# Kernel optimization log

Measured on AMD Instinct MI355X. Metric: run time of the kernel, lower is better.

Reference implementation:

```python
import jax, jax.numpy as jnp
import numpy as np

EPS = 1e-5
NUM_HEADS = 4


def _layer_norm(x, g, b):
    m = jnp.mean(x, axis=-1, keepdims=True)
    v = jnp.mean((x - m) ** 2, axis=-1, keepdims=True)
    return (x - m) / jnp.sqrt(v + EPS) * g + b


def setup_inputs() -> dict:
    key = jax.random.key(0)
    ks = jax.random.split(key, 32)
    B, N, ND, TD, L = 100000, 20, 128, 64, 2
    HD = 128  # num_heads * attention_dim
    CD = ND + TD  # 192
    s = 0.02
    inp = {
        "node_features": jax.random.normal(ks[0], (B, ND), jnp.float32),
        "neighbor_features": jax.random.normal(ks[1], (B, N, ND), jnp.float32),
        "node_times": jax.random.uniform(ks[2], (B,), jnp.float32),
        "neighbor_times": jax.random.uniform(ks[3], (B, N), jnp.float32),
        "time_freq": jax.random.normal(ks[4], (TD,), jnp.float32),
        "time_phase": jnp.zeros((TD,), jnp.float32),
        "Wq": jax.random.normal(ks[5], (L, CD, HD), jnp.float32) * s,
        "bq": jnp.zeros((L, HD), jnp.float32),
        "Wk": jax.random.normal(ks[6], (L, CD, HD), jnp.float32) * s,
        "bk": jnp.zeros((L, HD), jnp.float32),
        "Wv": jax.random.normal(ks[7], (L, CD, HD), jnp.float32) * s,
        "bv": jnp.zeros((L, HD), jnp.float32),
        "Wo": jax.random.normal(ks[8], (L, HD, ND), jnp.float32) * s,
        "bo": jnp.zeros((L, ND), jnp.float32),
        "W1": jax.random.normal(ks[9], (L, ND, 2 * ND), jnp.float32) * s,
        "b1": jnp.zeros((L, 2 * ND), jnp.float32),
        "W2": jax.random.normal(ks[10], (L, 2 * ND, ND), jnp.float32) * s,
        "b2": jnp.zeros((L, ND), jnp.float32),
        "g1": jnp.ones((L, ND), jnp.float32),
        "be1": jnp.zeros((L, ND), jnp.float32),
        "g2": jnp.ones((L, ND), jnp.float32),
        "be2": jnp.zeros((L, ND), jnp.float32),
        "Wc1": jax.random.normal(ks[11], (ND, ND // 2), jnp.float32) * s,
        "bc1": jnp.zeros((ND // 2,), jnp.float32),
        "Wc2": jax.random.normal(ks[12], (ND // 2, 1), jnp.float32) * s,
        "bc2": jnp.zeros((1,), jnp.float32),
        "mask": jax.random.randint(ks[13], (B, N), 0, 2, jnp.int32),
    }
    return inp


def reference(node_features, neighbor_features, node_times, neighbor_times,
              time_freq, time_phase, Wq, bq, Wk, bk, Wv, bv, Wo, bo,
              W1, b1, W2, b2, g1, be1, g2, be2, Wc1, bc1, Wc2, bc2, mask):
    L, _, HD = Wq.shape
    B, N, ND = neighbor_features.shape
    H = NUM_HEADS
    D = HD // H
    scale = 1.0 / np.sqrt(D).astype(np.float32)
    # time encodings (Bochner): cos(t * w + phi)
    tq = jnp.cos(node_times[:, None] * time_freq + time_phase)          # [B, TD]
    tk = jnp.cos(neighbor_times[..., None] * time_freq + time_phase)   # [B, N, TD]
    kcomb = jnp.concatenate([neighbor_features, tk], axis=-1)           # [B, N, CD]
    pad = (mask == 0)[:, None, :]                                       # [B, 1, N]
    x = node_features
    for l in range(L):
        qcomb = jnp.concatenate([x, tq], axis=-1)                       # [B, CD]
        q = (qcomb @ Wq[l] + bq[l]).reshape(B, H, D)
        k = (kcomb @ Wk[l] + bk[l]).reshape(B, N, H, D)
        v = (kcomb @ Wv[l] + bv[l]).reshape(B, N, H, D)
        scores = jnp.einsum('bhd,bnhd->bhn', q, k) * scale              # [B, H, N]
        scores = jnp.where(pad, jnp.float32(-1e9), scores)
        w = jax.nn.softmax(scores, axis=-1)
        a = jnp.einsum('bhn,bnhd->bhd', w, v).reshape(B, HD)
        attn = a @ Wo[l] + bo[l]                                        # [B, ND]
        x = _layer_norm(x + attn, g1[l], be1[l])
        ff = jax.nn.relu(x @ W1[l] + b1[l]) @ W2[l] + b2[l]
        x = _layer_norm(x + ff, g2[l], be2[l])
    h = jax.nn.relu(x @ Wc1 + bc1)
    return jax.nn.sigmoid(h @ Wc2 + bc2)                                # [B, 1]
```

## Files before the change

### kernel.cpp

```cpp
#include <hip/hip_runtime.h>

#define BB 100000
#define NN 20
#define ND 128
#define TD 64
#define CD 192
#define HD 128
#define NH 4
#define DH 32
#define NL 2

typedef __attribute__((ext_vector_type(8))) short bf16x8;
typedef __attribute__((ext_vector_type(4))) float f32x4;

static __device__ __forceinline__ float bf2f(unsigned short u) {
  return __uint_as_float(((unsigned)u) << 16);
}
static __device__ __forceinline__ unsigned short f2bf(float x) {
  unsigned b = __float_as_uint(x);
  return (unsigned short)((b + 0x7FFFu + ((b >> 16) & 1u)) >> 16);
}
static __device__ __forceinline__ bf16x8 load_a8(const float* p) {
  float4 a = *(const float4*)p, b = *(const float4*)(p + 4);
  bf16x8 r;
  r[0] = (short)f2bf(a.x); r[1] = (short)f2bf(a.y);
  r[2] = (short)f2bf(a.z); r[3] = (short)f2bf(a.w);
  r[4] = (short)f2bf(b.x); r[5] = (short)f2bf(b.y);
  r[6] = (short)f2bf(b.z); r[7] = (short)f2bf(b.w);
  return r;
}


__global__ __launch_bounds__(256) void conv_w(
    const float* __restrict__ Wq, const float* __restrict__ Wk,
    const float* __restrict__ Wv, const float* __restrict__ Wo,
    const float* __restrict__ W1, const float* __restrict__ W2,
    unsigned short* __restrict__ WF) {
  int t = blockIdx.x;
  int l = t / 304, tt = t % 304;
#pragma unroll
  for (int e = 0; e < 2; ++e) {
    int idx = threadIdx.x * 2 + e;
    int lane = idx >> 3, j = idx & 7;
    int wk = ((lane >> 4) << 3) + j;
    int c16 = lane & 15;
    float v;
    if (tt < 48) {
      int kt = tt >> 3, n2 = tt & 7;
      v = Wq[((size_t)l * CD + kt * 32 + wk) * HD + n2 * 16 + c16];
    } else if (tt < 96) {
      int t2 = tt - 48; int h = t2 / 12, n2 = t2 % 12;
      v = Wk[((size_t)l * CD + n2 * 16 + c16) * HD + h * 32 + wk];
    } else if (tt < 144) {
      int t2 = tt - 96; int h = t2 / 12, r2 = t2 % 12, kt = r2 >> 1, n2 = r2 & 1;
      v = Wv[((size_t)l * CD + kt * 32 + wk) * HD + h * 32 + n2 * 16 + c16];
    } else if (tt < 176) {
      int t2 = tt - 144; int kt = t2 >> 3, n2 = t2 & 7;
      v = Wo[((size_t)l * HD + kt * 32 + wk) * ND + n2 * 16 + c16];
    } else if (tt < 240) {
      int t2 = tt - 176; int kt = t2 >> 4, n2 = t2 & 15;
      v = W1[((size_t)l * ND + kt * 32 + wk) * (2 * ND) + n2 * 16 + c16];
    } else {
      int t2 = tt - 240; int kt = t2 >> 3, n2 = t2 & 7;
      v = W2[((size_t)l * 2 * ND + kt * 32 + wk) * ND + n2 * 16 + c16];
    }
    WF[(size_t)l * 155648 + (size_t)tt * 512 + idx] = f2bf(v);
  }
}

__global__ __launch_bounds__(256) void prep_tq(
    const float* __restrict__ ntime, const float* __restrict__ tf,
    const float* __restrict__ tp, float* __restrict__ tqf) {
  int i = blockIdx.x * 256 + threadIdx.x;
  int b = i >> 6, j = i & 63;
  tqf[i] = __cosf(ntime[b] * tf[j] + tp[j]);
}

__global__ __launch_bounds__(256) void prep_mb(const int* __restrict__ mask,
                                               unsigned* __restrict__ mb) {
  int e = blockIdx.x * 256 + threadIdx.x;
  if (e < BB) {
    unsigned m = 0;
    for (int n = 0; n < NN; ++n)
      m |= (mask[(size_t)e * NN + n] != 0 ? 1u : 0u) << n;
    mb[e] = m;
  }
}

__global__ __launch_bounds__(256) void gemm_yr(
    const float* __restrict__ A, const float* __restrict__ tqf,
    const unsigned short* __restrict__ WFl, const float* __restrict__ bq,
    unsigned short* __restrict__ rb) {
  __shared__ unsigned short ylds[16][136];
  const int tid = threadIdx.x;
  const int wv = tid >> 6, lane = tid & 63;
  const int m0 = blockIdx.x << 4;
  const int arow = m0 + (lane & 15);
  const int kgrp = (lane >> 4) << 3;
  {
    f32x4 acc[2];
    acc[0] = f32x4{0.f, 0.f, 0.f, 0.f};
    acc[1] = f32x4{0.f, 0.f, 0.f, 0.f};
    for (int kt = 0; kt < 6; ++kt) {
      bf16x8 af = (kt < 4)
                      ? load_a8(A + (size_t)arow * ND + kt * 32 + kgrp)
                      : load_a8(tqf + (size_t)arow * TD + (kt - 4) * 32 + kgrp);
#pragma unroll
      for (int i = 0; i < 2; ++i) {
        int nt = wv + 4 * i;
        bf16x8 bf = *(const bf16x8*)(WFl + (((size_t)(kt * 8 + nt)) << 9) +
                                     (lane << 3));
        acc[i] = __builtin_amdgcn_mfma_f32_16x16x32_bf16(af, bf, acc[i], 0, 0, 0);
      }
    }
    int lrow = (lane >> 4) << 2;
#pragma unroll
    for (int i = 0; i < 2; ++i) {
      int col = (wv + 4 * i) * 16 + (lane & 15);
      float bv = bq[col];
#pragma unroll
      for (int rr = 0; rr < 4; ++rr)
        ylds[lrow + rr][col] = f2bf(acc[i][rr] + bv);
    }
  }
  __syncthreads();
  {
    f32x4 acc[12];
#pragma unroll
    for (int i = 0; i < 12; ++i) acc[i] = f32x4{0.f, 0.f, 0.f, 0.f};
    bf16x8 af = *(const bf16x8*)&ylds[lane & 15][wv * 32 + kgrp];
    const unsigned short* B = WFl + 24576 + (size_t)wv * 12 * 512;
#pragma unroll
    for (int i = 0; i < 12; ++i) {
      bf16x8 bf = *(const bf16x8*)(B + (((size_t)i) << 9) + (lane << 3));
      acc[i] = __builtin_amdgcn_mfma_f32_16x16x32_bf16(af, bf, acc[i], 0, 0, 0);
    }
    int crow = m0 + ((lane >> 4) << 2);
#pragma unroll
    for (int i = 0; i < 12; ++i) {
      int col = wv * 192 + i * 16 + (lane & 15);
#pragma unroll
      for (int rr = 0; rr < 4; ++rr)
        rb[(size_t)(crow + rr) * 768 + col] = f2bf(acc[i][rr]);
    }
  }
}

__global__ __launch_bounds__(256) void gemm_aln1ff1(
    const unsigned short* __restrict__ u, const unsigned short* __restrict__ WFl,
    const float* __restrict__ bv, const float* __restrict__ bo,
    const float* __restrict__ res, const float* __restrict__ gamma,
    const float* __restrict__ beta, const float* __restrict__ b1,
    float* __restrict__ xout, unsigned short* __restrict__ h1b) {
  __shared__ unsigned short alds[16][136];
  __shared__ float Cs[16][132];
  const int tid = threadIdx.x;
  const int wv = tid >> 6, lane = tid & 63;
  const int m0 = blockIdx.x << 4;
  const int arow = m0 + (lane & 15);
  const int kgrp = (lane >> 4) << 3;
  {
    f32x4 acc0 = {0.f, 0.f, 0.f, 0.f}, acc1 = {0.f, 0.f, 0.f, 0.f};
    const unsigned short* B = WFl + 49152 + (size_t)wv * 12 * 512;
    for (int kt = 0; kt < 6; ++kt) {
      bf16x8 af = *(const bf16x8*)(u + (size_t)arow * 768 + wv * 192 +
                                   kt * 32 + kgrp);
      bf16x8 b0 = *(const bf16x8*)(B + (((size_t)(kt * 2 + 0)) << 9) + (lane << 3));
      bf16x8 b1f = *(const bf16x8*)(B + (((size_t)(kt * 2 + 1)) << 9) + (lane << 3));
      acc0 = __builtin_amdgcn_mfma_f32_16x16x32_bf16(af, b0, acc0, 0, 0, 0);
      acc1 = __builtin_amdgcn_mfma_f32_16x16x32_bf16(af, b1f, acc1, 0, 0, 0);
    }
    int lrow = (lane >> 4) << 2;
    int c0 = wv * 32 + (lane & 15), c1 = wv * 32 + 16 + (lane & 15);
    float bv0 = bv[c0], bv1 = bv[c1];
#pragma unroll
    for (int rr = 0; rr < 4; ++rr) {
      alds[lrow + rr][c0] = f2bf(acc0[rr] + bv0);
      alds[lrow + rr][c1] = f2bf(acc1[rr] + bv1);
    }
  }
  __syncthreads();
  {
    const int nt0 = wv, nt1 = wv + 4;
    f32x4 acc0 = {0.f, 0.f, 0.f, 0.f}, acc1 = {0.f, 0.f, 0.f, 0.f};
    for (int kt = 0; kt < 4; ++kt) {
      bf16x8 af = *(const bf16x8*)&alds[lane & 15][kt * 32 + kgrp];
      bf16x8 b0 = *(const bf16x8*)(WFl + 73728 +
                                   (((size_t)(kt * 8 + nt0)) << 9) + (lane << 3));
      bf16x8 b1f = *(const bf16x8*)(WFl + 73728 +
                                    (((size_t)(kt * 8 + nt1)) << 9) + (lane << 3));
      acc0 = __builtin_amdgcn_mfma_f32_16x16x32_bf16(af, b0, acc0, 0, 0, 0);
      acc1 = __builtin_amdgcn_mfma_f32_16x16x32_bf16(af, b1f, acc1, 0, 0, 0);
    }
    {
      int lrow = (lane >> 4) << 2;
      int c0 = nt0 * 16 + (lane & 15), c1 = nt1 * 16 + (lane & 15);
      float bv0 = bo[c0], bv1 = bo[c1];
#pragma unroll
      for (int rr = 0; rr < 4; ++rr) {
        Cs[lrow + rr][c0] = acc0[rr] + bv0;
        Cs[lrow + rr][c1] = acc1[rr] + bv1;
      }
    }
    __syncthreads();
#pragma unroll
    for (int rr = 0; rr < 4; ++rr) {
      int rw = wv * 4 + rr;
      size_t grow = (size_t)(m0 + rw) * ND;
      float y0 = Cs[rw][lane] + res[grow + lane];
      float y1 = Cs[rw][lane + 64] + res[grow + lane + 64];
      float s = y0 + y1, ss = y0 * y0 + y1 * y1;
#pragma unroll
      for (int off = 32; off > 0; off >>= 1) {
        s += __shfl_xor(s, off);
        ss += __shfl_xor(ss, off);
      }
      float mean = s * (1.f / ND);
      float var = ss * (1.f / ND) - mean * mean;
      float rstd = rsqrtf(var + 1e-5f);
      float x0 = (y0 - mean) * rstd * gamma[lane] + beta[lane];
      float x1 = (y1 - mean) * rstd * gamma[lane + 64] + beta[lane + 64];
      xout[grow + lane] = x0;
      xout[grow + lane + 64] = x1;
      Cs[rw][lane] = x0;
      Cs[rw][lane + 64] = x1;
    }
  }
  __syncthreads();
  {
    f32x4 acc[4];
#pragma unroll
    for (int i = 0; i < 4; ++i) acc[i] = f32x4{0.f, 0.f, 0.f, 0.f};
    for (int kt = 0; kt < 4; ++kt) {
      bf16x8 af = load_a8(&Cs[lane & 15][kt * 32 + kgrp]);
#pragma unroll
      for (int i = 0; i < 4; ++i) {
        int nt = wv + 4 * i;
        bf16x8 bf = *(const bf16x8*)(WFl + 90112 +
                                     (((size_t)(kt * 16 + nt)) << 9) + (lane << 3));
        acc[i] = __builtin_amdgcn_mfma_f32_16x16x32_bf16(af, bf, acc[i], 0, 0, 0);
      }
    }
    int crow = m0 + ((lane >> 4) << 2);
#pragma unroll
    for (int i = 0; i < 4; ++i) {
      int col = (wv + 4 * i) * 16 + (lane & 15);
      float bvv = b1[col];
#pragma unroll
      for (int rr = 0; rr < 4; ++rr)
        h1b[(size_t)(crow + rr) * (2 * ND) + col] =
            f2bf(fmaxf(acc[i][rr] + bvv, 0.f));
    }
  }
}

template <int ABF, int CLS>
__global__ __launch_bounds__(256) void gemm_ln(
    const void* __restrict__ A, int lda, int ktiles,
    const unsigned short* __restrict__ BF,
    const float* __restrict__ bias, const float* __restrict__ res,
    const float* __restrict__ gamma, const float* __restrict__ beta,
    float* __restrict__ xout,
    const float* __restrict__ Wc1, const float* __restrict__ bc1,
    const float* __restrict__ Wc2, const float* __restrict__ bc2,
    float* __restrict__ out) {
  __shared__ float Cs[16][132];
  __shared__ float hsh[CLS ? 16 : 1][64];
  const int tid = threadIdx.x;
  const int wv = tid >> 6, lane = tid & 63;
  const int m0 = blockIdx.x << 4;
  const int arow = m0 + (lane & 15);
  const int kgrp = (lane >> 4) << 3;
  const int nt0 = wv, nt1 = wv + 4;
  f32x4 acc0 = {0.f, 0.f, 0.f, 0.f}, acc1 = {0.f, 0.f, 0.f, 0.f};
  for (int kt = 0; kt < ktiles; ++kt) {
    bf16x8 af;
    if (ABF)
      af = *(const bf16x8*)((const unsigned short*)A + (size_t)arow * lda +
                            kt * 32 + kgrp);
    else
      af = load_a8((const float*)A + (size_t)arow * lda + kt * 32 + kgrp);
    bf16x8 b0 = *(const bf16x8*)(BF + (((size_t)(kt * 8 + nt0)) << 9) + (lane << 3));
    bf16x8 b1 = *(const bf16x8*)(BF + (((size_t)(kt * 8 + nt1)) << 9) + (lane << 3));
    acc0 = __builtin_amdgcn_mfma_f32_16x16x32_bf16(af, b0, acc0, 0, 0, 0);
    acc1 = __builtin_amdgcn_mfma_f32_16x16x32_bf16(af, b1, acc1, 0, 0, 0);
  }
  {
    const int lrow = (lane >> 4) << 2;
    int c0 = nt0 * 16 + (lane & 15), c1 = nt1 * 16 + (lane & 15);
    float bv0 = bias[c0], bv1 = bias[c1];
#pragma unroll
    for (int rr = 0; rr < 4; ++rr) {
      Cs[lrow + rr][c0] = acc0[rr] + bv0;
      Cs[lrow + rr][c1] = acc1[rr] + bv1;
    }
  }
  __syncthreads();
#pragma unroll
  for (int rr = 0; rr < 4; ++rr) {
    int rw = wv * 4 + rr;
    size_t grow = (size_t)(m0 + rw) * ND;
    float y0 = Cs[rw][lane] + res[grow + lane];
    float y1 = Cs[rw][lane + 64] + res[grow + lane + 64];
    float s = y0 + y1, ss = y0 * y0 + y1 * y1;
#pragma unroll
    for (int off = 32; off > 0; off >>= 1) {
      s += __shfl_xor(s, off);
      ss += __shfl_xor(ss, off);
    }
    float mean = s * (1.f / ND);
    float var = ss * (1.f / ND) - mean * mean;
    float rstd = rsqrtf(var + 1e-5f);
    float x0 = (y0 - mean) * rstd * gamma[lane] + beta[lane];
    float x1 = (y1 - mean) * rstd * gamma[lane + 64] + beta[lane + 64];
    if (CLS) {
      Cs[rw][lane] = x0;
      Cs[rw][lane + 64] = x1;
    } else {
      xout[grow + lane] = x0;
      xout[grow + lane + 64] = x1;
    }
  }
  if (CLS) {
    __syncthreads();
#pragma unroll
    for (int rep = 0; rep < 4; ++rep) {
      int idx = rep * 256 + tid;
      int row = idx >> 6, j = idx & 63;
      float a = 0.f;
      for (int c = 0; c < ND; ++c) a += Cs[row][c] * Wc1[c * 64 + j];
      hsh[row][j] = fmaxf(a + bc1[j], 0.f);
    }
    __syncthreads();
#pragma unroll
    for (int rr = 0; rr < 4; ++rr) {
      int row = wv * 4 + rr;
      float p = hsh[row][lane] * Wc2[lane];
#pragma unroll
      for (int off = 32; off > 0; off >>= 1) p += __shfl_xor(p, off);
      if (lane == 0)
        out[m0 + row] = 1.f / (1.f + expf(-(p + bc2[0])));
    }
  }
}

__global__ __launch_bounds__(256) void attn_b(
    const float* __restrict__ nbf, const float* __restrict__ nbt,
    const float* __restrict__ tf, const float* __restrict__ tp,
    const unsigned* __restrict__ mb, const unsigned short* __restrict__ r,
    unsigned short* __restrict__ u) {
  __shared__ __align__(16) unsigned short kcb[2][NN][200];
  __shared__ __align__(16) float rs[2][768];
  __shared__ __align__(16) float scs[2][NH][NN];
  __shared__ unsigned msks[2];
  const int tid = threadIdx.x;
  const size_t e0 = (size_t)blockIdx.x * 2;

  if (tid < 192) {
    uint4 v = *(const uint4*)(r + e0 * 768 + tid * 8);
    const unsigned short* pv = (const unsigned short*)&v;
    float* dst = &rs[0][0] + tid * 8;
#pragma unroll
    for (int k = 0; k < 8; ++k) dst[k] = bf2f(pv[k]);
  }
  for (int i = tid; i < 2 * NN * 32; i += 256) {
    int el = i / (NN * 32), rem = i % (NN * 32);
    int n = rem >> 5, cq = rem & 31;
    float4 v = *(const float4*)&nbf[((e0 + el) * NN + n) * ND + cq * 4];
    ushort4 o;
    o.x = f2bf(v.x); o.y = f2bf(v.y); o.z = f2bf(v.z); o.w = f2bf(v.w);
    *(ushort4*)&kcb[el][n][cq * 4] = o;
  }
  for (int i = tid; i < 2 * NN * 32; i += 256) {
    int el = i / (NN * 32), rem = i % (NN * 32);
    int n = rem >> 5, jp = (rem & 31) * 2;
    float t = nbt[(e0 + el) * NN + n];
    unsigned a = f2bf(__cosf(t * tf[jp] + tp[jp]));
    unsigned b = f2bf(__cosf(t * tf[jp + 1] + tp[jp + 1]));
    *(unsigned*)&kcb[el][n][ND + jp] = a | (b << 16);
  }
  if (tid < 2) msks[tid] = mb[e0 + tid];
  __syncthreads();
  if (tid < 2 * NH * NN) {
    int el = tid / (NH * NN), rem = tid % (NH * NN);
    int h = rem / NN, n = rem % NN;
    const float* rp = &rs[el][h * CD];
    const unsigned short* kp = &kcb[el][n][0];
    float acc = 0.f;
    for (int c = 0; c < CD; c += 4) {
      float4 rv = *(const float4*)&rp[c];
      ushort4 kv = *(const ushort4*)&kp[c];
      acc += rv.x * bf2f(kv.x) + rv.y * bf2f(kv.y) + rv.z * bf2f(kv.z) +
             rv.w * bf2f(kv.w);
    }
    scs[el][h][n] =
        ((msks[el] >> n) & 1u) ? acc * 0.17677669529663687f : -1e9f;
  }
  __syncthreads();
  if (tid < 2 * NH) {
    int el = tid >> 2, h = tid & 3;
    float mx = -3.4e38f;
#pragma unroll
    for (int n = 0; n < NN; ++n) mx = fmaxf(mx, scs[el][h][n]);
    float ev[NN], s = 0.f;
#pragma unroll
    for (int n = 0; n < NN; ++n) { ev[n] = __expf(scs[el][h][n] - mx); s += ev[n]; }
    float inv = 1.f / s;
#pragma unroll
    for (int n = 0; n < NN; ++n) scs[el][h][n] = ev[n] * inv;
  }
  __syncthreads();
  for (int i = tid; i < 2 * NH * (CD / 4); i += 256) {
    int el = i / (NH * 48), rem = i % (NH * 48);
    int h = rem / 48, cq = (rem % 48) * 4;
    float a0 = 0.f, a1 = 0.f, a2 = 0.f, a3 = 0.f;
#pragma unroll
    for (int n = 0; n < NN; ++n) {
      float w = scs[el][h][n];
      ushort4 kv = *(const ushort4*)&kcb[el][n][cq];
      a0 += w * bf2f(kv.x); a1 += w * bf2f(kv.y);
      a2 += w * bf2f(kv.z); a3 += w * bf2f(kv.w);
    }
    ushort4 o;
    o.x = f2bf(a0); o.y = f2bf(a1); o.z = f2bf(a2); o.w = f2bf(a3);
    *(ushort4*)&u[(e0 + el) * 768 + h * CD + cq] = o;
  }
}

#define G 2
#define T 256
#define KCS 196
#define RUS 772

__global__ __launch_bounds__(T, 4) void tgat_fused(
    const float* __restrict__ nf, const float* __restrict__ nbf,
    const float* __restrict__ nt, const float* __restrict__ nbt,
    const float* __restrict__ tf, const float* __restrict__ tp,
    const float* __restrict__ Wq, const float* __restrict__ bq,
    const float* __restrict__ Wk,
    const float* __restrict__ Wv, const float* __restrict__ bv,
    const float* __restrict__ Wo, const float* __restrict__ bo,
    const float* __restrict__ W1, const float* __restrict__ b1,
    const float* __restrict__ W2, const float* __restrict__ b2,
    const float* __restrict__ g1, const float* __restrict__ be1,
    const float* __restrict__ g2, const float* __restrict__ be2,
    const float* __restrict__ Wc1, const float* __restrict__ bc1,
    const float* __restrict__ Wc2, const float* __restrict__ bc2,
    const int* __restrict__ mask,
    float* __restrict__ out) {
  __shared__ __align__(16) unsigned short kc[G][NN][KCS];
  __shared__ __align__(16) float xs[G][ND];
  __shared__ __align__(16) float tqs[G][TD];
  __shared__ __align__(16) float ys[G][HD];
  __shared__ __align__(16) float rus[G][RUS];
  __shared__ __align__(16) float scs[G][NH][NN];
  __shared__ __align__(16) float h1s[G][2 * ND];
  __shared__ __align__(16) unsigned msks[G];
  float* asv = &h1s[0][0];
  const int tid = threadIdx.x;
  const int b0 = blockIdx.x * G;
  {
    int g = tid >> 7, j = tid & 127;
    xs[g][j] = nf[(b0 + g) * ND + j];
  }
  if (tid < G * TD) {
    int g = tid >> 6, j = tid & 63;
    tqs[g][j] = __cosf(nt[b0 + g] * tf[j] + tp[j]);
  }
  if (tid < G) {
    unsigned m = 0;
    for (int n = 0; n < NN; ++n)
      m |= (mask[(b0 + tid) * NN + n] != 0 ? 1u : 0u) << n;
    msks[tid] = m;
  }
  for (int idx = tid; idx < G * NN * (ND / 4); idx += T) {
    int g = idx / (NN * 32), rem = idx % (NN * 32);
    int n = rem >> 5, cq = rem & 31;
    float4 v = *(const float4*)&nbf[(((b0 + g) * NN + n) * ND) + cq * 4];
    ushort4 o;
    o.x = f2bf(v.x); o.y = f2bf(v.y); o.z = f2bf(v.z); o.w = f2bf(v.w);
    *(ushort4*)&kc[g][n][cq * 4] = o;
  }
  for (int idx = tid; idx < G * NN * TD; idx += T) {
    int g = idx / (NN * TD), rem = idx % (NN * TD);
    int n = rem >> 6, j = rem & 63;
    kc[g][n][ND + j] = f2bf(__cosf(nbt[(b0 + g) * NN + n] * tf[j] + tp[j]));
  }
  __syncthreads();
  const float scale = 0.17677669529663687f;
  for (int l = 0; l < NL; ++l) {
    {
      int g = tid >> 7, j = tid & 127;
      const float* wq = Wq + (l * CD) * HD + j;
      float acc = bq[l * HD + j];
      for (int c = 0; c < CD; c += 4) {
        float4 qv = (c < ND) ? *(const float4*)&xs[g][c]
                             : *(const float4*)&tqs[g][c - ND];
        acc += qv.x * wq[(c + 0) * HD] + qv.y * wq[(c + 1) * HD] +
               qv.z * wq[(c + 2) * HD] + qv.w * wq[(c + 3) * HD];
      }
      ys[g][j] = acc;
    }
    __syncthreads();
    for (int rep = 0; rep < 3; ++rep) {
      int i = rep * T + tid;
      int h = i / CD;
      int c2 = i - h * CD;
      const float* wk = Wk + (l * CD + c2) * HD + h * DH;
      const float* yp0 = &ys[0][h * DH];
      const float* yp1 = &ys[1][h * DH];
      float a0 = 0.f, a1 = 0.f;
#pragma unroll
      for (int d = 0; d < DH; d += 4) {
        float4 w4 = *(const float4*)&wk[d];
        float4 y0 = *(const float4*)&yp0[d];
        float4 y1 = *(const float4*)&yp1[d];
        a0 += y0.x * w4.x + y0.y * w4.y + y0.z * w4.z + y0.w * w4.w;
        a1 += y1.x * w4.x + y1.y * w4.y + y1.z * w4.z + y1.w * w4.w;
      }
      rus[0][i] = a0;
      rus[1][i] = a1;
    }
    __syncthreads();
    if (tid < G * NH * NN) {
      int g = tid / (NH * NN), rem = tid % (NH * NN);
      int h = rem / NN, n = rem % NN;
      const float* rp = &rus[g][h * CD];
      const unsigned short* kp = &kc[g][n][0];
      float acc = 0.f;
      for (int c = 0; c < CD; c += 4) {
        float4 rv = *(const float4*)&rp[c];
        ushort4 kv = *(const ushort4*)&kp[c];
        acc += rv.x * bf2f(kv.x) + rv.y * bf2f(kv.y) + rv.z * bf2f(kv.z) +
               rv.w * bf2f(kv.w);
      }
      scs[g][h][n] = ((msks[g] >> n) & 1u) ? acc * scale : -1e9f;
    }
    __syncthreads();
    if (tid < G * NH) {
      int g = tid / NH, h = tid % NH;
      float mx = -3.4e38f;
#pragma unroll
      for (int n = 0; n < NN; ++n) mx = fmaxf(mx, scs[g][h][n]);
      float ev[NN], s = 0.f;
#pragma unroll
      for (int n = 0; n < NN; ++n) { ev[n] = __expf(scs[g][h][n] - mx); s += ev[n]; }
      float inv = 1.f / s;
#pragma unroll
      for (int n = 0; n < NN; ++n) scs[g][h][n] = ev[n] * inv;
    }
    __syncthreads();
    for (int flat = tid; flat < G * NH * (CD / 4); flat += T) {
      int g = flat / (NH * 48), iq = flat % (NH * 48);
      int h = iq / 48, c = (iq % 48) * 4;
      const unsigned short* kp = &kc[g][0][0];
      float a0 = 0.f, a1 = 0.f, a2 = 0.f, a3 = 0.f;
#pragma unroll
      for (int n = 0; n < NN; ++n) {
        float w = scs[g][h][n];
        ushort4 kv = *(const ushort4*)&kp[n * KCS + c];
        a0 += w * bf2f(kv.x); a1 += w * bf2f(kv.y);
        a2 += w * bf2f(kv.z); a3 += w * bf2f(kv.w);
      }
      *(float4*)&rus[g][h * CD + c] = make_float4(a0, a1, a2, a3);
    }
    __syncthreads();
    {
      int j = tid & (HD - 1);
      int g = tid >> 7;
      int h = j >> 5;
      const float* wv = Wv + (l * CD) * HD + j;
      float acc = 0.f;
      for (int c = 0; c < CD; c += 4) {
        float4 uv = *(const float4*)&rus[g][h * CD + c];
        acc += uv.x * wv[(c + 0) * HD] + uv.y * wv[(c + 1) * HD] +
               uv.z * wv[(c + 2) * HD] + uv.w * wv[(c + 3) * HD];
      }
      asv[g * HD + j] = acc + bv[l * HD + j];
    }
    __syncthreads();
    {
      int j = tid & (ND - 1);
      int g = tid >> 7;
      const float* wo = Wo + (l * HD) * ND + j;
      float acc = 0.f;
      for (int c = 0; c < HD; c += 4) {
        float4 av = *(const float4*)&asv[g * HD + c];
        acc += av.x * wo[(c + 0) * ND] + av.y * wo[(c + 1) * ND] +
               av.z * wo[(c + 2) * ND] + av.w * wo[(c + 3) * ND];
      }
      rus[g][j] = acc + bo[l * ND + j];
    }
    __syncthreads();
    if (tid < G * 64) {
      int g = tid >> 6, lane = tid & 63;
      float y0 = xs[g][lane] + rus[g][lane];
      float y1 = xs[g][lane + 64] + rus[g][lane + 64];
      float s = y0 + y1, ss = y0 * y0 + y1 * y1;
#pragma unroll
      for (int off = 32; off > 0; off >>= 1) {
        s += __shfl_xor(s, off);
        ss += __shfl_xor(ss, off);
      }
      float mean = s * (1.f / ND);
      float var = ss * (1.f / ND) - mean * mean;
      float rstd = rsqrtf(var + 1e-5f);
      xs[g][lane] = (y0 - mean) * rstd * g1[l * ND + lane] + be1[l * ND + lane];
      xs[g][lane + 64] =
          (y1 - mean) * rstd * g1[l * ND + lane + 64] + be1[l * ND + lane + 64];
    }
    __syncthreads();
    {
      int j = tid;
      const float* w1p = W1 + (l * ND) * (2 * ND) + j;
      float acc0 = 0.f, acc1 = 0.f;
      for (int c = 0; c < ND; c += 4) {
        float w0 = w1p[(c + 0) * 2 * ND], wa = w1p[(c + 1) * 2 * ND],
              w2 = w1p[(c + 2) * 2 * ND], w3 = w1p[(c + 3) * 2 * ND];
        float4 x0 = *(const float4*)&xs[0][c];
        float4 x1 = *(const float4*)&xs[1][c];
        acc0 += x0.x * w0 + x0.y * wa + x0.z * w2 + x0.w * w3;
        acc1 += x1.x * w0 + x1.y * wa + x1.z * w2 + x1.w * w3;
      }
      float b1v = b1[l * 2 * ND + j];
      h1s[0][j] = fmaxf(acc0 + b1v, 0.f);
      h1s[1][j] = fmaxf(acc1 + b1v, 0.f);
    }
    __syncthreads();
    {
      int j = tid & (ND - 1);
      int g = tid >> 7;
      const float* w2p = W2 + (l * 2 * ND) * ND + j;
      float acc = 0.f;
      for (int c = 0; c < 2 * ND; c += 4) {
        float4 hv = *(const float4*)&h1s[g][c];
        acc += hv.x * w2p[(c + 0) * ND] + hv.y * w2p[(c + 1) * ND] +
               hv.z * w2p[(c + 2) * ND] + hv.w * w2p[(c + 3) * ND];
      }
      rus[g][j] = acc + b2[l * ND + j];
    }
    __syncthreads();
    if (tid < G * 64) {
      int g = tid >> 6, lane = tid & 63;
      float y0 = xs[g][lane] + rus[g][lane];
      float y1 = xs[g][lane + 64] + rus[g][lane + 64];
      float s = y0 + y1, ss = y0 * y0 + y1 * y1;
#pragma unroll
      for (int off = 32; off > 0; off >>= 1) {
        s += __shfl_xor(s, off);
        ss += __shfl_xor(ss, off);
      }
      float mean = s * (1.f / ND);
      float var = ss * (1.f / ND) - mean * mean;
      float rstd = rsqrtf(var + 1e-5f);
      xs[g][lane] = (y0 - mean) * rstd * g2[l * ND + lane] + be2[l * ND + lane];
      xs[g][lane + 64] =
          (y1 - mean) * rstd * g2[l * ND + lane + 64] + be2[l * ND + lane + 64];
    }
    __syncthreads();
  }
  if (tid < G * 64) {
    int j = tid & 63;
    int g = tid >> 6;
    const float* wc = Wc1 + j;
    float acc = 0.f;
    for (int c = 0; c < ND; c += 4) {
      float4 xv = *(const float4*)&xs[g][c];
      acc += xv.x * wc[(c + 0) * 64] + xv.y * wc[(c + 1) * 64] +
             xv.z * wc[(c + 2) * 64] + xv.w * wc[(c + 3) * 64];
    }
    ((float*)scs)[g * 64 + j] = fmaxf(acc + bc1[j], 0.f);
  }
  __syncthreads();
  if (tid < G * 64) {
    int g = tid >> 6, lane = tid & 63;
    float p = ((float*)scs)[g * 64 + lane] * Wc2[lane];
#pragma unroll
    for (int off = 32; off > 0; off >>= 1) p += __shfl_xor(p, off);
    if (lane == 0) {
      float z = p + bc2[0];
      out[b0 + g] = 1.f / (1.f + expf(-z));
    }
  }
}

extern "C" void kernel_launch(void* const* d_in, const int* in_sizes, int n_in,
                              void* d_out, int out_size, void* d_ws,
                              size_t ws_size, hipStream_t stream) {
  (void)in_sizes; (void)n_in; (void)out_size;
  const float* nf  = (const float*)d_in[0];
  const float* nbf = (const float*)d_in[1];
  const float* ntm = (const float*)d_in[2];
  const float* nbt = (const float*)d_in[3];
  const float* tf  = (const float*)d_in[4];
  const float* tp  = (const float*)d_in[5];
  const float* Wq  = (const float*)d_in[6];
  const float* bq  = (const float*)d_in[7];
  const float* Wk  = (const float*)d_in[8];
  const float* Wv  = (const float*)d_in[10];
  const float* bv  = (const float*)d_in[11];
  const float* Wo  = (const float*)d_in[12];
  const float* bo  = (const float*)d_in[13];
  const float* W1  = (const float*)d_in[14];
  const float* b1  = (const float*)d_in[15];
  const float* W2  = (const float*)d_in[16];
  const float* b2  = (const float*)d_in[17];
  const float* g1  = (const float*)d_in[18];
  const float* be1 = (const float*)d_in[19];
  const float* g2  = (const float*)d_in[20];
  const float* be2 = (const float*)d_in[21];
  const float* Wc1 = (const float*)d_in[22];
  const float* bc1 = (const float*)d_in[23];
  const float* Wc2 = (const float*)d_in[24];
  const float* bc2 = (const float*)d_in[25];
  const int* mask  = (const int*)d_in[26];
  float* out = (float*)d_out;

  const size_t NEED = 282622592ull;
  if (ws_size >= NEED) {
    char* w = (char*)d_ws;
    unsigned short* WF = (unsigned short*)w;
    unsigned* mb = (unsigned*)(w + 622592);
    float* tqf = (float*)(w + 1022592);
    unsigned short* rb = (unsigned short*)(w + 26622592);
    unsigned short* h1b = (unsigned short*)(w + 180222592);
    float* xfb = (float*)(w + 231422592);

    conv_w<<<608, 256, 0, stream>>>(Wq, Wk, Wv, Wo, W1, W2, WF);
    prep_tq<<<25000, 256, 0, stream>>>(ntm, tf, tp, tqf);
    prep_mb<<<(BB + 255) / 256, 256, 0, stream>>>(mask, mb);

    const float* xsrc = nf;
    for (int l = 0; l < NL; ++l) {
      const unsigned short* WFl = WF + (size_t)l * 155648;
      gemm_yr<<<6250, 256, 0, stream>>>(xsrc, tqf, WFl, bq + l * HD, rb);
      attn_b<<<50000, 256, 0, stream>>>(nbf, nbt, tf, tp, mb, rb, rb);
      gemm_aln1ff1<<<6250, 256, 0, stream>>>(
          rb, WFl, bv + l * HD, bo + l * ND, xsrc, g1 + l * ND, be1 + l * ND,
          b1 + l * 2 * ND, xfb, h1b);
      if (l == NL - 1)
        gemm_ln<1, 1><<<6250, 256, 0, stream>>>(
            h1b, 2 * ND, 8, WFl + 122880, b2 + l * ND, xfb, g2 + l * ND,
            be2 + l * ND, xfb, Wc1, bc1, Wc2, bc2, out);
      else
        gemm_ln<1, 0><<<6250, 256, 0, stream>>>(
            h1b, 2 * ND, 8, WFl + 122880, b2 + l * ND, xfb, g2 + l * ND,
            be2 + l * ND, xfb, nullptr, nullptr, nullptr, nullptr, nullptr);
      xsrc = xfb;
    }
  } else {
    tgat_fused<<<BB / G, T, 0, stream>>>(nf, nbf, ntm, nbt, tf, tp, Wq, bq, Wk,
                                         Wv, bv, Wo, bo, W1, b1, W2, b2, g1,
                                         be1, g2, be2, Wc1, bc1, Wc2, bc2,
                                         mask, out);
  }
}
```

Baseline: 1.288 ms.

## Fuse Q projection, neighbor attention and output/FFN1 into one layer kernel

Merges gemm_yr, attn_b and gemm_aln1ff1 into a single per-layer kernel. The 768-wide projected query buffer and the attention output now stay in shared memory instead of making round trips through global memory. The time-encoding buffer for nodes is also stored as bf16 rather than fp32, which shrinks the workspace. In exchange, the fused kernel uses far more shared memory and handles attention serially in four groups of four rows with many barriers. That may cut occupancy and reduce how well neighbor loads overlap with compute.

New measurement: 1.928 ms. +49.7%, slower.

```diff
diff --git a/kernel.cpp b/kernel.cpp
--- a/kernel.cpp
+++ b/kernel.cpp
@@ -70,10 +70,10 @@
 
 __global__ __launch_bounds__(256) void prep_tq(
     const float* __restrict__ ntime, const float* __restrict__ tf,
-    const float* __restrict__ tp, float* __restrict__ tqf) {
+    const float* __restrict__ tp, unsigned short* __restrict__ tqb) {
   int i = blockIdx.x * 256 + threadIdx.x;
   int b = i >> 6, j = i & 63;
-  tqf[i] = __cosf(ntime[b] * tf[j] + tp[j]);
+  tqb[i] = f2bf(__cosf(ntime[b] * tf[j] + tp[j]));
 }
 
 __global__ __launch_bounds__(256) void prep_mb(const int* __restrict__ mask,
@@ -87,16 +87,28 @@
   }
 }
 
-__global__ __launch_bounds__(256) void gemm_yr(
-    const float* __restrict__ A, const float* __restrict__ tqf,
+__global__ __launch_bounds__(256) void layer_fused(
+    const float* __restrict__ A, const unsigned short* __restrict__ tqb,
     const unsigned short* __restrict__ WFl, const float* __restrict__ bq,
-    unsigned short* __restrict__ rb) {
-  __shared__ unsigned short ylds[16][136];
+    const float* __restrict__ nbf, const float* __restrict__ nbt,
+    const float* __restrict__ tf, const float* __restrict__ tp,
+    const unsigned* __restrict__ mb, const float* __restrict__ bv,
+    const float* __restrict__ bo, const float* __restrict__ gamma,
+    const float* __restrict__ beta, const float* __restrict__ b1,
+    float* __restrict__ xout, unsigned short* __restrict__ h1b) {
+  __shared__ __align__(16) unsigned short ylds[16][136];
+  __shared__ __align__(16) unsigned short rlds[16][768];
+  __shared__ __align__(16) unsigned short kcb[4][NN][200];
+  __shared__ __align__(16) float scs[4][NH][NN];
+  __shared__ __align__(16) unsigned short alds[16][136];
+  __shared__ __align__(16) float Cs[16][132];
+  __shared__ unsigned msks[4];
   const int tid = threadIdx.x;
   const int wv = tid >> 6, lane = tid & 63;
   const int m0 = blockIdx.x << 4;
   const int arow = m0 + (lane & 15);
   const int kgrp = (lane >> 4) << 3;
+
   {
     f32x4 acc[2];
     acc[0] = f32x4{0.f, 0.f, 0.f, 0.f};
@@ -104,7 +116,8 @@
     for (int kt = 0; kt < 6; ++kt) {
       bf16x8 af = (kt < 4)
                       ? load_a8(A + (size_t)arow * ND + kt * 32 + kgrp)
-                      : load_a8(tqf + (size_t)arow * TD + (kt - 4) * 32 + kgrp);
+                      : *(const bf16x8*)(tqb + (size_t)arow * TD +
+                                         (kt - 4) * 32 + kgrp);
 #pragma unroll
       for (int i = 0; i < 2; ++i) {
         int nt = wv + 4 * i;
@@ -117,10 +130,10 @@
 #pragma unroll
     for (int i = 0; i < 2; ++i) {
       int col = (wv + 4 * i) * 16 + (lane & 15);
-      float bv = bq[col];
+      float bvv = bq[col];
 #pragma unroll
       for (int rr = 0; rr < 4; ++rr)
-        ylds[lrow + rr][col] = f2bf(acc[i][rr] + bv);
+        ylds[lrow + rr][col] = f2bf(acc[i][rr] + bvv);
     }
   }
   __syncthreads();
@@ -135,36 +148,88 @@
       bf16x8 bf = *(const bf16x8*)(B + (((size_t)i) << 9) + (lane << 3));
       acc[i] = __builtin_amdgcn_mfma_f32_16x16x32_bf16(af, bf, acc[i], 0, 0, 0);
     }
-    int crow = m0 + ((lane >> 4) << 2);
+    int lrow = (lane >> 4) << 2;
 #pragma unroll
     for (int i = 0; i < 12; ++i) {
       int col = wv * 192 + i * 16 + (lane & 15);
 #pragma unroll
       for (int rr = 0; rr < 4; ++rr)
-        rb[(size_t)(crow + rr) * 768 + col] = f2bf(acc[i][rr]);
-    }
-  }
-}
-
-__global__ __launch_bounds__(256) void gemm_aln1ff1(
-    const unsigned short* __restrict__ u, const unsigned short* __restrict__ WFl,
-    const float* __restrict__ bv, const float* __restrict__ bo,
-    const float* __restrict__ res, const float* __restrict__ gamma,
-    const float* __restrict__ beta, const float* __restrict__ b1,
-    float* __restrict__ xout, unsigned short* __restrict__ h1b) {
-  __shared__ unsigned short alds[16][136];
-  __shared__ float Cs[16][132];
-  const int tid = threadIdx.x;
-  const int wv = tid >> 6, lane = tid & 63;
-  const int m0 = blockIdx.x << 4;
-  const int arow = m0 + (lane & 15);
-  const int kgrp = (lane >> 4) << 3;
+        rlds[lrow + rr][col] = f2bf(acc[i][rr]);
+    }
+  }
+  __syncthreads();
+  for (int eg = 0; eg < 4; ++eg) {
+    const int r0 = eg * 4;
+    const size_t g0 = (size_t)(m0 + r0);
+    for (int i = tid; i < 4 * NN * 32; i += 256) {
+      int el = i / (NN * 32), rem = i % (NN * 32);
+      int n = rem >> 5, cq = rem & 31;
+      float4 v = *(const float4*)&nbf[((g0 + el) * NN + n) * ND + cq * 4];
+      ushort4 o;
+      o.x = f2bf(v.x); o.y = f2bf(v.y); o.z = f2bf(v.z); o.w = f2bf(v.w);
+      *(ushort4*)&kcb[el][n][cq * 4] = o;
+    }
+    for (int i = tid; i < 4 * NN * 32; i += 256) {
+      int el = i / (NN * 32), rem = i % (NN * 32);
+      int n = rem >> 5, jp = (rem & 31) * 2;
+      float t = nbt[(g0 + el) * NN + n];
+      unsigned a = f2bf(__cosf(t * tf[jp] + tp[jp]));
+      unsigned b = f2bf(__cosf(t * tf[jp + 1] + tp[jp + 1]));
+      *(unsigned*)&kcb[el][n][ND + jp] = a | (b << 16);
+    }
+    if (tid < 4) msks[tid] = mb[g0 + tid];
+    __syncthreads();
+    for (int idx = tid; idx < 4 * NH * NN; idx += 256) {
+      int el = idx / (NH * NN), rem = idx % (NH * NN);
+      int h = rem / NN, n = rem % NN;
+      const unsigned short* rp = &rlds[r0 + el][h * CD];
+      const unsigned short* kp = &kcb[el][n][0];
+      float acc = 0.f;
+      for (int c = 0; c < CD; c += 4) {
+        ushort4 rv = *(const ushort4*)&rp[c];
+        ushort4 kv = *(const ushort4*)&kp[c];
+        acc += bf2f(rv.x) * bf2f(kv.x) + bf2f(rv.y) * bf2f(kv.y) +
+               bf2f(rv.z) * bf2f(kv.z) + bf2f(rv.w) * bf2f(kv.w);
+      }
+      scs[el][h][n] =
+          ((msks[el] >> n) & 1u) ? acc * 0.17677669529663687f : -1e9f;
+    }
+    __syncthreads();
+    if (tid < 4 * NH) {
+      int el = tid >> 2, h = tid & 3;
+      float mx = -3.4e38f;
+#pragma unroll
+      for (int n = 0; n < NN; ++n) mx = fmaxf(mx, scs[el][h][n]);
+      float ev[NN], s = 0.f;
+#pragma unroll
+      for (int n = 0; n < NN; ++n) { ev[n] = __expf(scs[el][h][n] - mx); s += ev[n]; }
+      float inv = 1.f / s;
+#pragma unroll
+      for (int n = 0; n < NN; ++n) scs[el][h][n] = ev[n] * inv;
+    }
+    __syncthreads();
+    for (int i = tid; i < 4 * NH * 48; i += 256) {
+      int el = i / (NH * 48), rem = i % (NH * 48);
+      int h = rem / 48, cq = (rem % 48) * 4;
+      float a0 = 0.f, a1 = 0.f, a2 = 0.f, a3 = 0.f;
+#pragma unroll
+      for (int n = 0; n < NN; ++n) {
+        float w = scs[el][h][n];
+        ushort4 kv = *(const ushort4*)&kcb[el][n][cq];
+        a0 += w * bf2f(kv.x); a1 += w * bf2f(kv.y);
+        a2 += w * bf2f(kv.z); a3 += w * bf2f(kv.w);
+      }
+      ushort4 o;
+      o.x = f2bf(a0); o.y = f2bf(a1); o.z = f2bf(a2); o.w = f2bf(a3);
+      *(ushort4*)&rlds[r0 + el][h * CD + cq] = o;
+    }
+    __syncthreads();
+  }
   {
     f32x4 acc0 = {0.f, 0.f, 0.f, 0.f}, acc1 = {0.f, 0.f, 0.f, 0.f};
     const unsigned short* B = WFl + 49152 + (size_t)wv * 12 * 512;
     for (int kt = 0; kt < 6; ++kt) {
-      bf16x8 af = *(const bf16x8*)(u + (size_t)arow * 768 + wv * 192 +
-                                   kt * 32 + kgrp);
+      bf16x8 af = *(const bf16x8*)&rlds[lane & 15][wv * 192 + kt * 32 + kgrp];
       bf16x8 b0 = *(const bf16x8*)(B + (((size_t)(kt * 2 + 0)) << 9) + (lane << 3));
       bf16x8 b1f = *(const bf16x8*)(B + (((size_t)(kt * 2 + 1)) << 9) + (lane << 3));
       acc0 = __builtin_amdgcn_mfma_f32_16x16x32_bf16(af, b0, acc0, 0, 0, 0);
@@ -207,8 +272,8 @@
     for (int rr = 0; rr < 4; ++rr) {
       int rw = wv * 4 + rr;
       size_t grow = (size_t)(m0 + rw) * ND;
-      float y0 = Cs[rw][lane] + res[grow + lane];
-      float y1 = Cs[rw][lane + 64] + res[grow + lane + 64];
+      float y0 = Cs[rw][lane] + A[grow + lane];
+      float y1 = Cs[rw][lane + 64] + A[grow + lane + 64];
       float s = y0 + y1, ss = y0 * y0 + y1 * y1;
 #pragma unroll
       for (int off = 32; off > 0; off >>= 1) {
@@ -341,89 +406,6 @@
       if (lane == 0)
         out[m0 + row] = 1.f / (1.f + expf(-(p + bc2[0])));
     }
-  }
-}
-
-__global__ __launch_bounds__(256) void attn_b(
-    const float* __restrict__ nbf, const float* __restrict__ nbt,
-    const float* __restrict__ tf, const float* __restrict__ tp,
-    const unsigned* __restrict__ mb, const unsigned short* __restrict__ r,
-    unsigned short* __restrict__ u) {
-  __shared__ __align__(16) unsigned short kcb[2][NN][200];
-  __shared__ __align__(16) float rs[2][768];
-  __shared__ __align__(16) float scs[2][NH][NN];
-  __shared__ unsigned msks[2];
-  const int tid = threadIdx.x;
-  const size_t e0 = (size_t)blockIdx.x * 2;
-
-  if (tid < 192) {
-    uint4 v = *(const uint4*)(r + e0 * 768 + tid * 8);
-    const unsigned short* pv = (const unsigned short*)&v;
-    float* dst = &rs[0][0] + tid * 8;
-#pragma unroll
-    for (int k = 0; k < 8; ++k) dst[k] = bf2f(pv[k]);
-  }
-  for (int i = tid; i < 2 * NN * 32; i += 256) {
-    int el = i / (NN * 32), rem = i % (NN * 32);
-    int n = rem >> 5, cq = rem & 31;
-    float4 v = *(const float4*)&nbf[((e0 + el) * NN + n) * ND + cq * 4];
-    ushort4 o;
-    o.x = f2bf(v.x); o.y = f2bf(v.y); o.z = f2bf(v.z); o.w = f2bf(v.w);
-    *(ushort4*)&kcb[el][n][cq * 4] = o;
-  }
-  for (int i = tid; i < 2 * NN * 32; i += 256) {
-    int el = i / (NN * 32), rem = i % (NN * 32);
-    int n = rem >> 5, jp = (rem & 31) * 2;
-    float t = nbt[(e0 + el) * NN + n];
-    unsigned a = f2bf(__cosf(t * tf[jp] + tp[jp]));
-    unsigned b = f2bf(__cosf(t * tf[jp + 1] + tp[jp + 1]));
-    *(unsigned*)&kcb[el][n][ND + jp] = a | (b << 16);
-  }
-  if (tid < 2) msks[tid] = mb[e0 + tid];
-  __syncthreads();
-  if (tid < 2 * NH * NN) {
-    int el = tid / (NH * NN), rem = tid % (NH * NN);
-    int h = rem / NN, n = rem % NN;
-    const float* rp = &rs[el][h * CD];
-    const unsigned short* kp = &kcb[el][n][0];
-    float acc = 0.f;
-    for (int c = 0; c < CD; c += 4) {
-      float4 rv = *(const float4*)&rp[c];
-      ushort4 kv = *(const ushort4*)&kp[c];
-      acc += rv.x * bf2f(kv.x) + rv.y * bf2f(kv.y) + rv.z * bf2f(kv.z) +
-             rv.w * bf2f(kv.w);
-    }
-    scs[el][h][n] =
-        ((msks[el] >> n) & 1u) ? acc * 0.17677669529663687f : -1e9f;
-  }
-  __syncthreads();
-  if (tid < 2 * NH) {
-    int el = tid >> 2, h = tid & 3;
-    float mx = -3.4e38f;
-#pragma unroll
-    for (int n = 0; n < NN; ++n) mx = fmaxf(mx, scs[el][h][n]);
-    float ev[NN], s = 0.f;
-#pragma unroll
-    for (int n = 0; n < NN; ++n) { ev[n] = __expf(scs[el][h][n] - mx); s += ev[n]; }
-    float inv = 1.f / s;
-#pragma unroll
-    for (int n = 0; n < NN; ++n) scs[el][h][n] = ev[n] * inv;
-  }
-  __syncthreads();
-  for (int i = tid; i < 2 * NH * (CD / 4); i += 256) {
-    int el = i / (NH * 48), rem = i % (NH * 48);
-    int h = rem / 48, cq = (rem % 48) * 4;
-    float a0 = 0.f, a1 = 0.f, a2 = 0.f, a3 = 0.f;
-#pragma unroll
-    for (int n = 0; n < NN; ++n) {
-      float w = scs[el][h][n];
-      ushort4 kv = *(const ushort4*)&kcb[el][n][cq];
-      a0 += w * bf2f(kv.x); a1 += w * bf2f(kv.y);
-      a2 += w * bf2f(kv.z); a3 += w * bf2f(kv.w);
-    }
-    ushort4 o;
-    o.x = f2bf(a0); o.y = f2bf(a1); o.z = f2bf(a2); o.w = f2bf(a3);
-    *(ushort4*)&u[(e0 + el) * 768 + h * CD + cq] = o;
   }
 }
 
@@ -716,28 +698,25 @@
   const int* mask  = (const int*)d_in[26];
   float* out = (float*)d_out;
 
-  const size_t NEED = 282622592ull;
+  const size_t NEED = 116222592ull;
   if (ws_size >= NEED) {
     char* w = (char*)d_ws;
     unsigned short* WF = (unsigned short*)w;
     unsigned* mb = (unsigned*)(w + 622592);
-    float* tqf = (float*)(w + 1022592);
-    unsigned short* rb = (unsigned short*)(w + 26622592);
-    unsigned short* h1b = (unsigned short*)(w + 180222592);
-    float* xfb = (float*)(w + 231422592);
+    unsigned short* tqb = (unsigned short*)(w + 1022592);
+    unsigned short* h1b = (unsigned short*)(w + 13822592);
+    float* xfb = (float*)(w + 65022592);
 
     conv_w<<<608, 256, 0, stream>>>(Wq, Wk, Wv, Wo, W1, W2, WF);
-    prep_tq<<<25000, 256, 0, stream>>>(ntm, tf, tp, tqf);
+    prep_tq<<<25000, 256, 0, stream>>>(ntm, tf, tp, tqb);
     prep_mb<<<(BB + 255) / 256, 256, 0, stream>>>(mask, mb);
 
     const float* xsrc = nf;
     for (int l = 0; l < NL; ++l) {
       const unsigned short* WFl = WF + (size_t)l * 155648;
-      gemm_yr<<<6250, 256, 0, stream>>>(xsrc, tqf, WFl, bq + l * HD, rb);
-      attn_b<<<50000, 256, 0, stream>>>(nbf, nbt, tf, tp, mb, rb, rb);
-      gemm_aln1ff1<<<6250, 256, 0, stream>>>(
-          rb, WFl, bv + l * HD, bo + l * ND, xsrc, g1 + l * ND, be1 + l * ND,
-          b1 + l * 2 * ND, xfb, h1b);
+      layer_fused<<<6250, 256, 0, stream>>>(
+          xsrc, tqb, WFl, bq + l * HD, nbf, nbt, tf, tp, mb, bv + l * HD,
+          bo + l * ND, g1 + l * ND, be1 + l * ND, b1 + l * 2 * ND, xfb, h1b);
       if (l == NL - 1)
         gemm_ln<1, 1><<<6250, 256, 0, stream>>>(
             h1b, 2 * ND, 8, WFl + 122880, b2 + l * ND, xfb, g2 + l * ND,
```
